# Performance work log

Hardware: AMD Instinct MI355X
Metric: run time of the kernel (lower is better)

## Reference

```python
import jax, jax.numpy as jnp
import numpy as np

EMBED_DIM = 768
N_HEADS = 12
TIME_RATIO = 0.5
HEAD_DIM = EMBED_DIM // N_HEADS          # 64
T_HEAD = int(HEAD_DIM * TIME_RATIO)      # 32 time dims per head
T_DIM = T_HEAD * N_HEADS                 # 384 time dims overall
EPS = 1e-5


def _ln(v, g, b):
    m = jnp.mean(v, axis=-1, keepdims=True)
    var = jnp.mean((v - m) ** 2, axis=-1, keepdims=True)
    return (v - m) * jax.lax.rsqrt(var + EPS) * g + b


def minkowski_ln(x, g_t, b_t, g_s, b_s):
    # normalize time-like and space-like channel groups separately
    xt, xs = x[..., :T_DIM], x[..., T_DIM:]
    return jnp.concatenate([_ln(xt, g_t, b_t), _ln(xs, g_s, b_s)], axis=-1)


def lorentz_attention(x, Wq, bq, Wk, bk, Wv, bv, Wo, bo):
    B, S, D = x.shape
    def heads(W, b):
        return (x @ W + b).reshape(B, S, N_HEADS, HEAD_DIM).transpose(0, 2, 1, 3)
    q, k, v = heads(Wq, bq), heads(Wk, bk), heads(Wv, bv)
    # Minkowski metric signature (-,...,-,+,...,+) within each head
    eta = jnp.concatenate([-jnp.ones((T_HEAD,), x.dtype), jnp.ones((HEAD_DIM - T_HEAD,), x.dtype)])
    logits = jnp.einsum('bhqd,bhkd->bhqk', q * eta, k) / np.sqrt(HEAD_DIM).astype(np.float32)
    attn = jax.nn.softmax(logits, axis=-1)
    o = jnp.einsum('bhqk,bhkd->bhqd', attn, v)
    o = o.transpose(0, 2, 1, 3).reshape(B, S, D)
    return o @ Wo + bo


def setup_inputs() -> dict:
    key = jax.random.key(0)
    ks = jax.random.split(key, 16)
    D, H4 = EMBED_DIM, EMBED_DIM * 4
    s = 0.02
    inp = {
        'x': jax.random.normal(ks[0], (2, 2048, D), jnp.float32),
        'Wq': jax.random.normal(ks[1], (D, D), jnp.float32) * s, 'bq': jnp.zeros((D,), jnp.float32),
        'Wk': jax.random.normal(ks[2], (D, D), jnp.float32) * s, 'bk': jnp.zeros((D,), jnp.float32),
        'Wv': jax.random.normal(ks[3], (D, D), jnp.float32) * s, 'bv': jnp.zeros((D,), jnp.float32),
        'Wo': jax.random.normal(ks[4], (D, D), jnp.float32) * s, 'bo': jnp.zeros((D,), jnp.float32),
        'g1t': jnp.ones((T_DIM,), jnp.float32), 'b1t': jnp.zeros((T_DIM,), jnp.float32),
        'g1s': jnp.ones((D - T_DIM,), jnp.float32), 'b1s': jnp.zeros((D - T_DIM,), jnp.float32),
        'W1': jax.random.normal(ks[5], (D, H4), jnp.float32) * s, 'bb1': jnp.zeros((H4,), jnp.float32),
        'W2': jax.random.normal(ks[6], (H4, D), jnp.float32) * s, 'bb2': jnp.zeros((D,), jnp.float32),
        'g2t': jnp.ones((T_DIM,), jnp.float32), 'b2t': jnp.zeros((T_DIM,), jnp.float32),
        'g2s': jnp.ones((D - T_DIM,), jnp.float32), 'b2s': jnp.zeros((D - T_DIM,), jnp.float32),
    }
    return inp


def reference(x, Wq, bq, Wk, bk, Wv, bv, Wo, bo,
              g1t, b1t, g1s, b1s, W1, bb1, W2, bb2,
              g2t, b2t, g2s, b2s):
    a = lorentz_attention(x, Wq, bq, Wk, bk, Wv, bv, Wo, bo)
    x = minkowski_ln(x + a, g1t, b1t, g1s, b1s)
    h = jax.nn.gelu(x @ W1 + bb1) @ W2 + bb2
    x = minkowski_ln(x + h, g2t, b2t, g2s, b2s)
    return x
```

## Files before the change

kernel.cpp:

```cpp
#include <hip/hip_runtime.h>
#include <cstddef>
#include <cstdint>

#define D_EMB  768
#define NHEAD  12
#define HDIM   64
#define THEAD  32
#define SEQ    2048
#define BATCH  2
#define NROW   (BATCH*SEQ)
#define HID4   3072

typedef unsigned short u16;
typedef __bf16 bf16x8 __attribute__((ext_vector_type(8)));
typedef float  f32x4  __attribute__((ext_vector_type(4)));
typedef unsigned short u16x8 __attribute__((ext_vector_type(8)));

__device__ __forceinline__ u16 f2bf(float f) {
    unsigned u = __builtin_bit_cast(unsigned, f);
    return (u16)((u + 0x7FFFu + ((u >> 16) & 1u)) >> 16);
}
__device__ __forceinline__ float bf2f(u16 h) {
    return __builtin_bit_cast(float, (unsigned)h << 16);
}

__device__ __forceinline__ void gload_lds16(const void* g, void* l) {
    __builtin_amdgcn_global_load_lds(
        reinterpret_cast<const __attribute__((address_space(1))) void*>(
            reinterpret_cast<uintptr_t>(g)),
        reinterpret_cast<__attribute__((address_space(3))) void*>(
            (uint32_t)reinterpret_cast<uintptr_t>(l)),
        16, 0, 0);
}

__global__ __launch_bounds__(256)
void cast_bf16(const float* __restrict__ in, u16* __restrict__ out, int n)
{
    const int i = (blockIdx.x * 256 + threadIdx.x) * 8;
    if (i >= n) return;
    const float4 a = *reinterpret_cast<const float4*>(in + i);
    const float4 b = *reinterpret_cast<const float4*>(in + i + 4);
    u16x8 h;
    h[0] = f2bf(a.x); h[1] = f2bf(a.y); h[2] = f2bf(a.z); h[3] = f2bf(a.w);
    h[4] = f2bf(b.x); h[5] = f2bf(b.y); h[6] = f2bf(b.z); h[7] = f2bf(b.w);
    *reinterpret_cast<u16x8*>(out + i) = h;
}

__global__ __launch_bounds__(256)
void concat_bias(const float* __restrict__ bq, const float* __restrict__ bk,
                 const float* __restrict__ bv, float* __restrict__ dst)
{
    const int i = blockIdx.x * 256 + threadIdx.x;
    if (i >= 2304) return;
    dst[i] = i < 768 ? bq[i] : (i < 1536 ? bk[i - 768] : bv[i - 1536]);
}

__global__ __launch_bounds__(256)
void transpose_cast(const float* __restrict__ W, u16* __restrict__ WT,
                    int K, int M)
{
    __shared__ float t[32][33];
    const int m0 = blockIdx.x * 32, k0 = blockIdx.y * 32;
    const int tx = threadIdx.x & 31, ty = threadIdx.x >> 5;
#pragma unroll
    for (int i = 0; i < 32; i += 8)
        t[ty + i][tx] = W[(size_t)(k0 + ty + i) * M + m0 + tx];
    __syncthreads();
#pragma unroll
    for (int i = 0; i < 32; i += 8)
        WT[(size_t)(m0 + ty + i) * K + k0 + tx] = f2bf(t[tx][ty + i]);
}

__global__ __launch_bounds__(256)
void transpose_cast4(const float* __restrict__ W0, const float* __restrict__ W1_,
                     const float* __restrict__ W2_, const float* __restrict__ W3_,
                     u16* __restrict__ WT)
{
    __shared__ float t[32][33];
    const int z = blockIdx.z;
    const float* W = z == 0 ? W0 : z == 1 ? W1_ : z == 2 ? W2_ : W3_;
    const int m0 = blockIdx.x * 32, k0 = blockIdx.y * 32;
    const int tx = threadIdx.x & 31, ty = threadIdx.x >> 5;
#pragma unroll
    for (int i = 0; i < 32; i += 8)
        t[ty + i][tx] = W[(size_t)(k0 + ty + i) * 768 + m0 + tx];
    __syncthreads();
#pragma unroll
    for (int i = 0; i < 32; i += 8)
        WT[(size_t)(z * 768 + m0 + ty + i) * 768 + k0 + tx] = f2bf(t[tx][ty + i]);
}

template<int EPI>
__global__ __launch_bounds__(256)
void gemm_bf16(const u16* __restrict__ A, const u16* __restrict__ B,
               const float* __restrict__ bias, void* __restrict__ Cp,
               u16* __restrict__ VTp, int K, int N)
{
    __shared__ u16 As[2][128 * 32];
    __shared__ u16 Bs[2][128 * 32];
    const int tid  = threadIdx.x;
    const int lane = tid & 63;
    const int w    = tid >> 6;
    const int m0 = blockIdx.x * 128, n0 = blockIdx.y * 128;
    const int wr = (w >> 1) << 6, wc = (w & 1) << 6;

    const int seg0 = (w << 11) + lane * 16;
    const int row0 = seg0 >> 6, cb0 = (seg0 & 63) >> 1;
    const int seg1 = seg0 + 1024;
    const int row1 = seg1 >> 6, cb1 = (seg1 & 63) >> 1;
    const u16* a0 = A + (size_t)(m0 + row0) * K + cb0;
    const u16* a1 = A + (size_t)(m0 + row1) * K + cb1;
    const u16* b0 = B + (size_t)(n0 + row0) * K + cb0;
    const u16* b1 = B + (size_t)(n0 + row1) * K + cb1;
    const int lo0 = (w * 2 + 0) << 9;
    const int lo1 = (w * 2 + 1) << 9;

    int aIdx[4], bIdx[4];
#pragma unroll
    for (int i = 0; i < 4; ++i) {
        aIdx[i] = (wr + i * 16 + (lane & 15)) * 32 + ((lane >> 4) << 3);
        bIdx[i] = (wc + i * 16 + (lane & 15)) * 32 + ((lane >> 4) << 3);
    }

    f32x4 acc[4][4];
#pragma unroll
    for (int i = 0; i < 4; ++i)
#pragma unroll
        for (int j = 0; j < 4; ++j)
#pragma unroll
            for (int q = 0; q < 4; ++q) acc[i][j][q] = 0.f;

    gload_lds16(a0, &As[0][lo0]);
    gload_lds16(a1, &As[0][lo1]);
    gload_lds16(b0, &Bs[0][lo0]);
    gload_lds16(b1, &Bs[0][lo1]);
    __syncthreads();

    int cur = 0;
    for (int k0 = 0; k0 < K; k0 += 32) {
        if (k0 + 32 < K) {
            gload_lds16(a0 + k0 + 32, &As[cur ^ 1][lo0]);
            gload_lds16(a1 + k0 + 32, &As[cur ^ 1][lo1]);
            gload_lds16(b0 + k0 + 32, &Bs[cur ^ 1][lo0]);
            gload_lds16(b1 + k0 + 32, &Bs[cur ^ 1][lo1]);
        }
        bf16x8 af[4], bv[4];
#pragma unroll
        for (int i = 0; i < 4; ++i)
            af[i] = *reinterpret_cast<const bf16x8*>(&As[cur][aIdx[i]]);
#pragma unroll
        for (int j = 0; j < 4; ++j)
            bv[j] = *reinterpret_cast<const bf16x8*>(&Bs[cur][bIdx[j]]);
#pragma unroll
        for (int i = 0; i < 4; ++i)
#pragma unroll
            for (int j = 0; j < 4; ++j)
                acc[i][j] = __builtin_amdgcn_mfma_f32_16x16x32_bf16(
                    af[i], bv[j], acc[i][j], 0, 0, 0);
        __syncthreads();
        cur ^= 1;
    }

#pragma unroll
    for (int i = 0; i < 4; ++i) {
#pragma unroll
        for (int q = 0; q < 4; ++q) {
            const int row = m0 + wr + i * 16 + ((lane >> 4) << 2) + q;
#pragma unroll
            for (int j = 0; j < 4; ++j) {
                const int col = n0 + wc + j * 16 + (lane & 15);
                float v = acc[i][j][q] + bias[col];
                if (EPI == 2) {
                    const float u3 = v * v * v;
                    v = 0.5f * v * (1.f + tanhf(0.7978845608028654f *
                                                (v + 0.044715f * u3)));
                }
                if (EPI == 0) {
                    ((float*)Cp)[(size_t)row * N + col] = v;
                } else if (EPI == 2) {
                    ((u16*)Cp)[(size_t)row * N + col] = f2bf(v);
                } else {
                    if (n0 < 1536) {
                        ((u16*)Cp)[(size_t)row * 1536 + col] = f2bf(v);
                    } else {
                        const int c2 = col - 1536;
                        const int hh = c2 >> 6, dd = c2 & 63;
                        const int bb = row >> 11, tok = row & 2047;
                        VTp[((size_t)(bb * NHEAD + hh) * HDIM + dd) * SEQ + tok]
                            = f2bf(v);
                    }
                }
            }
        }
    }
}

__global__ __launch_bounds__(256)
void gemm_n64(const u16* __restrict__ A, const u16* __restrict__ B,
              const float* __restrict__ bias, float* __restrict__ C,
              int K, int N)
{
    __shared__ u16 As[2][64 * 32];
    __shared__ u16 Bs[2][128 * 32];
    const int tid  = threadIdx.x;
    const int lane = tid & 63;
    const int w    = tid >> 6;
    const int l15  = lane & 15;
    const int g    = lane >> 4;
    const int m0 = blockIdx.x * 64, n0 = blockIdx.y * 128;

    const int segA = (w << 10) + lane * 16;
    const int rowA = segA >> 6, cbA = (segA & 63) >> 1;
    const u16* aP = A + (size_t)(m0 + rowA) * K + cbA;
    const int loA = w << 9;
    const int seg0 = (w << 11) + lane * 16;
    const int row0 = seg0 >> 6, cb0 = (seg0 & 63) >> 1;
    const int seg1 = seg0 + 1024;
    const int row1 = seg1 >> 6, cb1 = (seg1 & 63) >> 1;
    const u16* b0 = B + (size_t)(n0 + row0) * K + cb0;
    const u16* b1 = B + (size_t)(n0 + row1) * K + cb1;
    const int lo0 = w << 10, lo1 = (w << 10) + 512;

    int aIdx[4], bIdx[2];
#pragma unroll
    for (int i = 0; i < 4; ++i) aIdx[i] = (i * 16 + l15) * 32 + (g << 3);
#pragma unroll
    for (int j = 0; j < 2; ++j) bIdx[j] = ((w << 5) + j * 16 + l15) * 32 + (g << 3);

    f32x4 acc[4][2];
#pragma unroll
    for (int i = 0; i < 4; ++i)
#pragma unroll
        for (int j = 0; j < 2; ++j)
#pragma unroll
            for (int q = 0; q < 4; ++q) acc[i][j][q] = 0.f;

    gload_lds16(aP, &As[0][loA]);
    gload_lds16(b0, &Bs[0][lo0]);
    gload_lds16(b1, &Bs[0][lo1]);
    __syncthreads();

    int cur = 0;
    for (int k0 = 0; k0 < K; k0 += 32) {
        if (k0 + 32 < K) {
            gload_lds16(aP + k0 + 32, &As[cur ^ 1][loA]);
            gload_lds16(b0 + k0 + 32, &Bs[cur ^ 1][lo0]);
            gload_lds16(b1 + k0 + 32, &Bs[cur ^ 1][lo1]);
        }
        bf16x8 af[4], bv[2];
#pragma unroll
        for (int i = 0; i < 4; ++i)
            af[i] = *reinterpret_cast<const bf16x8*>(&As[cur][aIdx[i]]);
#pragma unroll
        for (int j = 0; j < 2; ++j)
            bv[j] = *reinterpret_cast<const bf16x8*>(&Bs[cur][bIdx[j]]);
#pragma unroll
        for (int i = 0; i < 4; ++i)
#pragma unroll
            for (int j = 0; j < 2; ++j)
                acc[i][j] = __builtin_amdgcn_mfma_f32_16x16x32_bf16(
                    af[i], bv[j], acc[i][j], 0, 0, 0);
        __syncthreads();
        cur ^= 1;
    }

#pragma unroll
    for (int i = 0; i < 4; ++i) {
#pragma unroll
        for (int q = 0; q < 4; ++q) {
            const int row = m0 + i * 16 + (g << 2) + q;
#pragma unroll
            for (int j = 0; j < 2; ++j) {
                const int col = n0 + (w << 5) + j * 16 + l15;
                C[(size_t)row * N + col] = acc[i][j][q] + bias[col];
            }
        }
    }
}

__global__ __launch_bounds__(256)
void attn_mfma(const u16* __restrict__ QK, const u16* __restrict__ VT,
               u16* __restrict__ O)
{
    __shared__ u16 Ks[2][64 * 64];
    __shared__ u16 Vs[2][64 * 64];
    __shared__ u16 Ps[64 * 72];

    const int tid  = threadIdx.x;
    const int lane = tid & 63;
    const int w    = tid >> 6;
    const int l15  = lane & 15;
    const int g    = lane >> 4;
    const int bh   = blockIdx.x;
    const int b    = bh / NHEAD, h = bh % NHEAD;
    const int q0   = blockIdx.y * 64;
    const int bS   = b * SEQ;

    bf16x8 aq[2];
    {
        const u16* Qg = QK + (size_t)(bS + q0 + (w << 4) + l15) * 1536 + h * HDIM;
#pragma unroll
        for (int kk = 0; kk < 2; ++kk) {
            u16x8 hq = *reinterpret_cast<const u16x8*>(Qg + kk * 32 + g * 8);
            if (kk == 0) {
#pragma unroll
                for (int j = 0; j < 8; ++j) hq[j] ^= 0x8000u;
            }
            aq[kk] = __builtin_bit_cast(bf16x8, hq);
        }
    }

    const int rl = lane >> 3;
    const int cs = (((lane & 7) ^ rl) << 3);
    const u16* pK = QK + (size_t)(bS + 16 * w + rl) * 1536 + 768 + h * HDIM + cs;
    const u16* pV = VT + ((size_t)(b * NHEAD + h) * HDIM + 16 * w + rl) * SEQ + cs;

    int swz[2];
#pragma unroll
    for (int kk = 0; kk < 2; ++kk)
        swz[kk] = ((kk * 4 + g) ^ (l15 & 7)) << 3;

    f32x4 accO[4];
#pragma unroll
    for (int n = 0; n < 4; ++n)
#pragma unroll
        for (int q = 0; q < 4; ++q) accO[n][q] = 0.f;
    float psum[4] = {0.f, 0.f, 0.f, 0.f};

#define ATTN_STAGE(c, kt)                                                   \
    do {                                                                    \
        u16* dK = &Ks[c][w * 1024];                                         \
        u16* dV = &Vs[c][w * 1024];                                         \
        gload_lds16(pK + (size_t)(kt) * 1536,     dK);                      \
        gload_lds16(pK + (size_t)((kt) + 8) * 1536, dK + 512);              \
        gload_lds16(pV + (kt),            dV);                              \
        gload_lds16(pV + (kt) + 8 * SEQ,  dV + 512);                        \
    } while (0)

    ATTN_STAGE(0, 0);
    __syncthreads();
    int cur = 0;

    for (int kt = 0; kt < SEQ; kt += 64) {
        if (kt + 64 < SEQ) ATTN_STAGE(cur ^ 1, kt + 64);

        f32x4 sac[4];
#pragma unroll
        for (int n = 0; n < 4; ++n) {
#pragma unroll
            for (int q = 0; q < 4; ++q) sac[n][q] = 0.f;
#pragma unroll
            for (int kk = 0; kk < 2; ++kk) {
                const bf16x8 bk = *reinterpret_cast<const bf16x8*>(
                    &Ks[cur][(n * 16 + l15) * 64 + swz[kk]]);
                sac[n] = __builtin_amdgcn_mfma_f32_16x16x32_bf16(
                    aq[kk], bk, sac[n], 0, 0, 0);
            }
        }

#pragma unroll
        for (int r4 = 0; r4 < 4; ++r4) {
            const int prow = (w << 4) + (g << 2) + r4;
#pragma unroll
            for (int n = 0; n < 4; ++n) {
                const float sv =
                    __builtin_amdgcn_exp2f(sac[n][r4] * 0.18033688011112042f);
                psum[r4] += sv;
                *(__bf16*)&Ps[prow * 72 + n * 16 + l15] = (__bf16)sv;
            }
        }

        bf16x8 pa[2];
#pragma unroll
        for (int kk = 0; kk < 2; ++kk)
            pa[kk] = *reinterpret_cast<const bf16x8*>(
                &Ps[((w << 4) + l15) * 72 + kk * 32 + g * 8]);
#pragma unroll
        for (int n = 0; n < 4; ++n) {
#pragma unroll
            for (int kk = 0; kk < 2; ++kk) {
                const bf16x8 bv = *reinterpret_cast<const bf16x8*>(
                    &Vs[cur][(n * 16 + l15) * 64 + swz[kk]]);
                accO[n] = __builtin_amdgcn_mfma_f32_16x16x32_bf16(
                    pa[kk], bv, accO[n], 0, 0, 0);
            }
        }
        __syncthreads();
        cur ^= 1;
    }

#pragma unroll
    for (int r4 = 0; r4 < 4; ++r4) {
        float ps = psum[r4];
#pragma unroll
        for (int off = 1; off < 16; off <<= 1)
            ps += __shfl_xor(ps, off, 16);
        const float inv = 1.f / ps;
        const int qr = q0 + (w << 4) + (g << 2) + r4;
#pragma unroll
        for (int n = 0; n < 4; ++n)
            O[(size_t)(bS + qr) * D_EMB + h * HDIM + n * 16 + l15]
                = f2bf(accO[n][r4] * inv);
    }
#undef ATTN_STAGE
}

__global__ __launch_bounds__(256)
void mink_ln(const float* __restrict__ X, const float* __restrict__ R,
             const float* __restrict__ gt, const float* __restrict__ bt,
             const float* __restrict__ gs, const float* __restrict__ bs,
             float* __restrict__ Out, u16* __restrict__ OutB, int nrows)
{
    const int wid  = (int)((blockIdx.x * 256 + threadIdx.x) >> 6);
    const int lane = threadIdx.x & 63;
    const int row  = wid >> 1, half = wid & 1;
    if (row >= nrows) return;

    const float* g  = half ? gs : gt;
    const float* bb = half ? bs : bt;
    const size_t base = (size_t)row * D_EMB + half * 384;

    float v[6];
    float sum = 0.f;
#pragma unroll
    for (int i = 0; i < 6; ++i) {
        const float t = X[base + i * 64 + lane] + R[base + i * 64 + lane];
        v[i] = t; sum += t;
    }
#pragma unroll
    for (int off = 32; off; off >>= 1) sum += __shfl_xor(sum, off);
    const float mean = sum * (1.f / 384.f);

    float ss = 0.f;
#pragma unroll
    for (int i = 0; i < 6; ++i) { const float d = v[i] - mean; ss += d * d; }
#pragma unroll
    for (int off = 32; off; off >>= 1) ss += __shfl_xor(ss, off);
    const float rstd = rsqrtf(ss * (1.f / 384.f) + 1e-5f);

#pragma unroll
    for (int i = 0; i < 6; ++i) {
        const int e = i * 64 + lane;
        const float o = (v[i] - mean) * rstd * g[e] + bb[e];
        Out[base + e] = o;
        if (OutB) OutB[base + e] = f2bf(o);
    }
}

extern "C" void kernel_launch(void* const* d_in, const int* in_sizes, int n_in,
                              void* d_out, int out_size, void* d_ws, size_t ws_size,
                              hipStream_t stream)
{
    const float* x   = (const float*)d_in[0];
    const float* Wq  = (const float*)d_in[1];
    const float* bq  = (const float*)d_in[2];
    const float* Wk  = (const float*)d_in[3];
    const float* bk  = (const float*)d_in[4];
    const float* Wv  = (const float*)d_in[5];
    const float* bv  = (const float*)d_in[6];
    const float* Wo  = (const float*)d_in[7];
    const float* bo  = (const float*)d_in[8];
    const float* g1t = (const float*)d_in[9];
    const float* b1t = (const float*)d_in[10];
    const float* g1s = (const float*)d_in[11];
    const float* b1s = (const float*)d_in[12];
    const float* W1  = (const float*)d_in[13];
    const float* bb1 = (const float*)d_in[14];
    const float* W2  = (const float*)d_in[15];
    const float* bb2 = (const float*)d_in[16];
    const float* g2t = (const float*)d_in[17];
    const float* b2t = (const float*)d_in[18];
    const float* g2s = (const float*)d_in[19];
    const float* b2s = (const float*)d_in[20];
    float* out = (float*)d_out;

    const size_t ND = (size_t)NROW * D_EMB;
    u16* WqkvoT = (u16*)d_ws;
    u16* W1T = WqkvoT + 2359296;
    u16* W2T = W1T + 2359296;
    u16* xb  = W2T + 2359296;
    u16* QKb = xb + ND;
    u16* VTb = QKb + (size_t)NROW * 1536;
    u16* Ab  = VTb + ND;
    u16* Hb  = QKb;
    float* AoF  = (float*)(Ab + ND);
    float* bqkv = AoF;
    float* X1   = AoF + ND;

    const dim3 blk(256);

    cast_bf16<<<1536, blk, 0, stream>>>(x, xb, (int)ND);
    concat_bias<<<9, blk, 0, stream>>>(bq, bk, bv, bqkv);
    transpose_cast4<<<dim3(24, 24, 4), blk, 0, stream>>>(Wq, Wk, Wv, Wo, WqkvoT);
    transpose_cast<<<dim3(96, 24), blk, 0, stream>>>(W1, W1T, 768, 3072);
    transpose_cast<<<dim3(24, 96), blk, 0, stream>>>(W2, W2T, 3072, 768);

    gemm_bf16<3><<<dim3(32, 18), blk, 0, stream>>>(xb, WqkvoT, bqkv, QKb, VTb,
                                                   768, 2304);
    attn_mfma<<<dim3(BATCH * NHEAD, SEQ / 64), blk, 0, stream>>>(QKb, VTb, Ab);

    gemm_n64<<<dim3(64, 6), blk, 0, stream>>>(Ab, WqkvoT + (size_t)2304 * 768,
                                              bo, AoF, 768, 768);
    mink_ln<<<2048, blk, 0, stream>>>(x, AoF, g1t, b1t, g1s, b1s, X1, xb, NROW);
    gemm_bf16<2><<<dim3(32, 24), blk, 0, stream>>>(xb, W1T, bb1, Hb, nullptr,
                                                   768, 3072);
    gemm_n64<<<dim3(64, 6), blk, 0, stream>>>(Hb, W2T, bb2, AoF, 3072, 768);
    mink_ln<<<2048, blk, 0, stream>>>(X1, AoF, g2t, b2t, g2s, b2s, out, nullptr, NROW);
}
```

Before: 209.7 us.

## Merge prep kernels and give attention waves two query tiles each

Five preprocessing launches (x cast, bias concat, three weight transposes) become one kernel that dispatches on block index. The attention kernel now runs 2 waves per 64-query block, each wave owning 32 query rows. Each K/V fragment loaded from LDS therefore feeds two MFMAs. P is written as packed 4-element stores, and the QKV GEMM writes V^T with the token order permuted within each 64-token group to match that layout. Costs are higher register pressure from doubled accumulators and fewer waves per block to hide latency.

```diff
diff --git a/kernel.cpp b/kernel.cpp
--- a/kernel.cpp
+++ b/kernel.cpp
@@ -20,9 +20,6 @@
     unsigned u = __builtin_bit_cast(unsigned, f);
     return (u16)((u + 0x7FFFu + ((u >> 16) & 1u)) >> 16);
 }
-__device__ __forceinline__ float bf2f(u16 h) {
-    return __builtin_bit_cast(float, (unsigned)h << 16);
-}
 
 __device__ __forceinline__ void gload_lds16(const void* g, void* l) {
     __builtin_amdgcn_global_load_lds(
@@ -33,34 +30,11 @@
         16, 0, 0);
 }
 
-__global__ __launch_bounds__(256)
-void cast_bf16(const float* __restrict__ in, u16* __restrict__ out, int n)
-{
-    const int i = (blockIdx.x * 256 + threadIdx.x) * 8;
-    if (i >= n) return;
-    const float4 a = *reinterpret_cast<const float4*>(in + i);
-    const float4 b = *reinterpret_cast<const float4*>(in + i + 4);
-    u16x8 h;
-    h[0] = f2bf(a.x); h[1] = f2bf(a.y); h[2] = f2bf(a.z); h[3] = f2bf(a.w);
-    h[4] = f2bf(b.x); h[5] = f2bf(b.y); h[6] = f2bf(b.z); h[7] = f2bf(b.w);
-    *reinterpret_cast<u16x8*>(out + i) = h;
-}
-
-__global__ __launch_bounds__(256)
-void concat_bias(const float* __restrict__ bq, const float* __restrict__ bk,
-                 const float* __restrict__ bv, float* __restrict__ dst)
-{
-    const int i = blockIdx.x * 256 + threadIdx.x;
-    if (i >= 2304) return;
-    dst[i] = i < 768 ? bq[i] : (i < 1536 ? bk[i - 768] : bv[i - 1536]);
-}
-
-__global__ __launch_bounds__(256)
-void transpose_cast(const float* __restrict__ W, u16* __restrict__ WT,
-                    int K, int M)
-{
-    __shared__ float t[32][33];
-    const int m0 = blockIdx.x * 32, k0 = blockIdx.y * 32;
+__device__ __forceinline__ void tcast(float (*t)[33], const float* __restrict__ W,
+                                      u16* __restrict__ WT, int K, int M,
+                                      int mt, int kt)
+{
+    const int m0 = mt * 32, k0 = kt * 32;
     const int tx = threadIdx.x & 31, ty = threadIdx.x >> 5;
 #pragma unroll
     for (int i = 0; i < 32; i += 8)
@@ -72,22 +46,40 @@
 }
 
 __global__ __launch_bounds__(256)
-void transpose_cast4(const float* __restrict__ W0, const float* __restrict__ W1_,
-                     const float* __restrict__ W2_, const float* __restrict__ W3_,
-                     u16* __restrict__ WT)
+void prep(const float* __restrict__ Wq, const float* __restrict__ Wk,
+          const float* __restrict__ Wv, const float* __restrict__ Wo,
+          const float* __restrict__ W1, const float* __restrict__ W2,
+          const float* __restrict__ bq, const float* __restrict__ bk,
+          const float* __restrict__ bv, const float* __restrict__ x,
+          u16* __restrict__ WqkvoT, u16* __restrict__ W1T,
+          u16* __restrict__ W2T, u16* __restrict__ xb,
+          float* __restrict__ bqkv)
 {
     __shared__ float t[32][33];
-    const int z = blockIdx.z;
-    const float* W = z == 0 ? W0 : z == 1 ? W1_ : z == 2 ? W2_ : W3_;
-    const int m0 = blockIdx.x * 32, k0 = blockIdx.y * 32;
-    const int tx = threadIdx.x & 31, ty = threadIdx.x >> 5;
-#pragma unroll
-    for (int i = 0; i < 32; i += 8)
-        t[ty + i][tx] = W[(size_t)(k0 + ty + i) * 768 + m0 + tx];
-    __syncthreads();
-#pragma unroll
-    for (int i = 0; i < 32; i += 8)
-        WT[(size_t)(z * 768 + m0 + ty + i) * 768 + k0 + tx] = f2bf(t[tx][ty + i]);
+    const int bid = blockIdx.x;
+    if (bid < 2304) {
+        const int z = bid / 576, r = bid % 576;
+        const float* W = z == 0 ? Wq : z == 1 ? Wk : z == 2 ? Wv : Wo;
+        tcast(t, W, WqkvoT + (size_t)z * 768 * 768, 768, 768, r % 24, r / 24);
+    } else if (bid < 4608) {
+        const int r = bid - 2304;
+        tcast(t, W1, W1T, 768, 3072, r % 96, r / 96);
+    } else if (bid < 6912) {
+        const int r = bid - 4608;
+        tcast(t, W2, W2T, 3072, 768, r % 24, r / 24);
+    } else if (bid < 8448) {
+        const int i = (bid - 6912) * 2048 + threadIdx.x * 8;
+        const float4 a = *reinterpret_cast<const float4*>(x + i);
+        const float4 b = *reinterpret_cast<const float4*>(x + i + 4);
+        u16x8 h;
+        h[0] = f2bf(a.x); h[1] = f2bf(a.y); h[2] = f2bf(a.z); h[3] = f2bf(a.w);
+        h[4] = f2bf(b.x); h[5] = f2bf(b.y); h[6] = f2bf(b.z); h[7] = f2bf(b.w);
+        *reinterpret_cast<u16x8*>(xb + i) = h;
+    } else {
+        const int i = (bid - 8448) * 256 + threadIdx.x;
+        if (i < 2304)
+            bqkv[i] = i < 768 ? bq[i] : (i < 1536 ? bk[i - 768] : bv[i - 1536]);
+    }
 }
 
 template<int EPI>
@@ -174,10 +166,6 @@
                     const float u3 = v * v * v;
                     v = 0.5f * v * (1.f + tanhf(0.7978845608028654f *
                                                 (v + 0.044715f * u3)));
-                }
-                if (EPI == 0) {
-                    ((float*)Cp)[(size_t)row * N + col] = v;
-                } else if (EPI == 2) {
                     ((u16*)Cp)[(size_t)row * N + col] = f2bf(v);
                 } else {
                     if (n0 < 1536) {
@@ -186,8 +174,10 @@
                         const int c2 = col - 1536;
                         const int hh = c2 >> 6, dd = c2 & 63;
                         const int bb = row >> 11, tok = row & 2047;
-                        VTp[((size_t)(bb * NHEAD + hh) * HDIM + dd) * SEQ + tok]
-                            = f2bf(v);
+                        const int t = tok & 63;
+                        const int p = ((t & 15) << 2) | (t >> 4);
+                        VTp[((size_t)(bb * NHEAD + hh) * HDIM + dd) * SEQ
+                            + (tok & ~63) + p] = f2bf(v);
                     }
                 }
             }
@@ -278,7 +268,7 @@
     }
 }
 
-__global__ __launch_bounds__(256)
+__global__ __launch_bounds__(128)
 void attn_mfma(const u16* __restrict__ QK, const u16* __restrict__ VT,
                u16* __restrict__ O)
 {
@@ -296,9 +286,11 @@
     const int q0   = blockIdx.y * 64;
     const int bS   = b * SEQ;
 
-    bf16x8 aq[2];
-    {
-        const u16* Qg = QK + (size_t)(bS + q0 + (w << 4) + l15) * 1536 + h * HDIM;
+    bf16x8 aq[2][2];
+#pragma unroll
+    for (int qb = 0; qb < 2; ++qb) {
+        const u16* Qg = QK + (size_t)(bS + q0 + w * 32 + qb * 16 + l15) * 1536
+                        + h * HDIM;
 #pragma unroll
         for (int kk = 0; kk < 2; ++kk) {
             u16x8 hq = *reinterpret_cast<const u16x8*>(Qg + kk * 32 + g * 8);
@@ -306,35 +298,38 @@
 #pragma unroll
                 for (int j = 0; j < 8; ++j) hq[j] ^= 0x8000u;
             }
-            aq[kk] = __builtin_bit_cast(bf16x8, hq);
+            aq[qb][kk] = __builtin_bit_cast(bf16x8, hq);
         }
     }
 
     const int rl = lane >> 3;
-    const int cs = (((lane & 7) ^ rl) << 3);
-    const u16* pK = QK + (size_t)(bS + 16 * w + rl) * 1536 + 768 + h * HDIM + cs;
-    const u16* pV = VT + ((size_t)(b * NHEAD + h) * HDIM + 16 * w + rl) * SEQ + cs;
+    const int cs = ((lane & 7) ^ rl) << 3;
+    const u16* pK = QK + (size_t)(bS + w * 32 + rl) * 1536 + 768 + h * HDIM + cs;
+    const u16* pV = VT + ((size_t)(b * NHEAD + h) * HDIM + w * 32 + rl) * SEQ + cs;
 
     int swz[2];
 #pragma unroll
     for (int kk = 0; kk < 2; ++kk)
         swz[kk] = ((kk * 4 + g) ^ (l15 & 7)) << 3;
 
-    f32x4 accO[4];
-#pragma unroll
-    for (int n = 0; n < 4; ++n)
-#pragma unroll
-        for (int q = 0; q < 4; ++q) accO[n][q] = 0.f;
-    float psum[4] = {0.f, 0.f, 0.f, 0.f};
-
-#define ATTN_STAGE(c, kt)                                                   \
-    do {                                                                    \
-        u16* dK = &Ks[c][w * 1024];                                         \
-        u16* dV = &Vs[c][w * 1024];                                         \
-        gload_lds16(pK + (size_t)(kt) * 1536,     dK);                      \
-        gload_lds16(pK + (size_t)((kt) + 8) * 1536, dK + 512);              \
-        gload_lds16(pV + (kt),            dV);                              \
-        gload_lds16(pV + (kt) + 8 * SEQ,  dV + 512);                        \
+    f32x4 accO[2][4];
+#pragma unroll
+    for (int qb = 0; qb < 2; ++qb)
+#pragma unroll
+        for (int n = 0; n < 4; ++n)
+#pragma unroll
+            for (int q = 0; q < 4; ++q) accO[qb][n][q] = 0.f;
+    float psum[2][4] = {};
+
+#define ATTN_STAGE(c, kt)                                                    \
+    do {                                                                     \
+        u16* dK = &Ks[c][w * 2048];                                          \
+        u16* dV = &Vs[c][w * 2048];                                          \
+        _Pragma("unroll")                                                    \
+        for (int i = 0; i < 4; ++i) {                                        \
+            gload_lds16(pK + (size_t)((kt) + 8 * i) * 1536, dK + 512 * i);   \
+            gload_lds16(pV + (size_t)(8 * i) * SEQ + (kt),  dV + 512 * i);   \
+        }                                                                    \
     } while (0)
 
     ATTN_STAGE(0, 0);
@@ -344,64 +339,83 @@
     for (int kt = 0; kt < SEQ; kt += 64) {
         if (kt + 64 < SEQ) ATTN_STAGE(cur ^ 1, kt + 64);
 
-        f32x4 sac[4];
-#pragma unroll
-        for (int n = 0; n < 4; ++n) {
-#pragma unroll
-            for (int q = 0; q < 4; ++q) sac[n][q] = 0.f;
-#pragma unroll
-            for (int kk = 0; kk < 2; ++kk) {
-                const bf16x8 bk = *reinterpret_cast<const bf16x8*>(
+        bf16x8 bk[4][2];
+#pragma unroll
+        for (int n = 0; n < 4; ++n)
+#pragma unroll
+            for (int kk = 0; kk < 2; ++kk)
+                bk[n][kk] = *reinterpret_cast<const bf16x8*>(
                     &Ks[cur][(n * 16 + l15) * 64 + swz[kk]]);
-                sac[n] = __builtin_amdgcn_mfma_f32_16x16x32_bf16(
-                    aq[kk], bk, sac[n], 0, 0, 0);
+
+        f32x4 sac[2][4];
+#pragma unroll
+        for (int qb = 0; qb < 2; ++qb)
+#pragma unroll
+            for (int n = 0; n < 4; ++n) {
+#pragma unroll
+                for (int q = 0; q < 4; ++q) sac[qb][n][q] = 0.f;
+#pragma unroll
+                for (int kk = 0; kk < 2; ++kk)
+                    sac[qb][n] = __builtin_amdgcn_mfma_f32_16x16x32_bf16(
+                        aq[qb][kk], bk[n][kk], sac[qb][n], 0, 0, 0);
             }
-        }
-
-#pragma unroll
-        for (int r4 = 0; r4 < 4; ++r4) {
-            const int prow = (w << 4) + (g << 2) + r4;
-#pragma unroll
-            for (int n = 0; n < 4; ++n) {
-                const float sv =
-                    __builtin_amdgcn_exp2f(sac[n][r4] * 0.18033688011112042f);
-                psum[r4] += sv;
-                *(__bf16*)&Ps[prow * 72 + n * 16 + l15] = (__bf16)sv;
+
+#pragma unroll
+        for (int qb = 0; qb < 2; ++qb)
+#pragma unroll
+            for (int r4 = 0; r4 < 4; ++r4) {
+                const int prow = w * 32 + qb * 16 + g * 4 + r4;
+                ushort4 pk4;
+                float sv0 = __builtin_amdgcn_exp2f(sac[qb][0][r4] * 0.18033688011112042f);
+                float sv1 = __builtin_amdgcn_exp2f(sac[qb][1][r4] * 0.18033688011112042f);
+                float sv2 = __builtin_amdgcn_exp2f(sac[qb][2][r4] * 0.18033688011112042f);
+                float sv3 = __builtin_amdgcn_exp2f(sac[qb][3][r4] * 0.18033688011112042f);
+                psum[qb][r4] += sv0 + sv1 + sv2 + sv3;
+                pk4.x = f2bf(sv0); pk4.y = f2bf(sv1);
+                pk4.z = f2bf(sv2); pk4.w = f2bf(sv3);
+                *reinterpret_cast<ushort4*>(&Ps[prow * 72 + (l15 << 2)]) = pk4;
             }
-        }
-
-        bf16x8 pa[2];
-#pragma unroll
-        for (int kk = 0; kk < 2; ++kk)
-            pa[kk] = *reinterpret_cast<const bf16x8*>(
-                &Ps[((w << 4) + l15) * 72 + kk * 32 + g * 8]);
-#pragma unroll
-        for (int n = 0; n < 4; ++n) {
-#pragma unroll
-            for (int kk = 0; kk < 2; ++kk) {
-                const bf16x8 bv = *reinterpret_cast<const bf16x8*>(
+
+        bf16x8 bv[4][2];
+#pragma unroll
+        for (int n = 0; n < 4; ++n)
+#pragma unroll
+            for (int kk = 0; kk < 2; ++kk)
+                bv[n][kk] = *reinterpret_cast<const bf16x8*>(
                     &Vs[cur][(n * 16 + l15) * 64 + swz[kk]]);
-                accO[n] = __builtin_amdgcn_mfma_f32_16x16x32_bf16(
-                    pa[kk], bv, accO[n], 0, 0, 0);
-            }
+#pragma unroll
+        for (int qb = 0; qb < 2; ++qb) {
+            bf16x8 pa[2];
+#pragma unroll
+            for (int kk = 0; kk < 2; ++kk)
+                pa[kk] = *reinterpret_cast<const bf16x8*>(
+                    &Ps[(w * 32 + qb * 16 + l15) * 72 + kk * 32 + g * 8]);
+#pragma unroll
+            for (int n = 0; n < 4; ++n)
+#pragma unroll
+                for (int kk = 0; kk < 2; ++kk)
+                    accO[qb][n] = __builtin_amdgcn_mfma_f32_16x16x32_bf16(
+                        pa[kk], bv[n][kk], accO[qb][n], 0, 0, 0);
         }
         __syncthreads();
         cur ^= 1;
     }
 
 #pragma unroll
-    for (int r4 = 0; r4 < 4; ++r4) {
-        float ps = psum[r4];
-#pragma unroll
-        for (int off = 1; off < 16; off <<= 1)
-            ps += __shfl_xor(ps, off, 16);
-        const float inv = 1.f / ps;
-        const int qr = q0 + (w << 4) + (g << 2) + r4;
-#pragma unroll
-        for (int n = 0; n < 4; ++n)
-            O[(size_t)(bS + qr) * D_EMB + h * HDIM + n * 16 + l15]
-                = f2bf(accO[n][r4] * inv);
-    }
+    for (int qb = 0; qb < 2; ++qb)
+#pragma unroll
+        for (int r4 = 0; r4 < 4; ++r4) {
+            float ps = psum[qb][r4];
+#pragma unroll
+            for (int off = 1; off < 16; off <<= 1)
+                ps += __shfl_xor(ps, off, 16);
+            const float inv = 1.f / ps;
+            const int qr = q0 + w * 32 + qb * 16 + g * 4 + r4;
+#pragma unroll
+            for (int n = 0; n < 4; ++n)
+                O[(size_t)(bS + qr) * D_EMB + h * HDIM + n * 16 + l15]
+                    = f2bf(accO[qb][n][r4] * inv);
+        }
 #undef ATTN_STAGE
 }
 
@@ -489,15 +503,12 @@
 
     const dim3 blk(256);
 
-    cast_bf16<<<1536, blk, 0, stream>>>(x, xb, (int)ND);
-    concat_bias<<<9, blk, 0, stream>>>(bq, bk, bv, bqkv);
-    transpose_cast4<<<dim3(24, 24, 4), blk, 0, stream>>>(Wq, Wk, Wv, Wo, WqkvoT);
-    transpose_cast<<<dim3(96, 24), blk, 0, stream>>>(W1, W1T, 768, 3072);
-    transpose_cast<<<dim3(24, 96), blk, 0, stream>>>(W2, W2T, 3072, 768);
+    prep<<<8457, blk, 0, stream>>>(Wq, Wk, Wv, Wo, W1, W2, bq, bk, bv, x,
+                                   WqkvoT, W1T, W2T, xb, bqkv);
 
     gemm_bf16<3><<<dim3(32, 18), blk, 0, stream>>>(xb, WqkvoT, bqkv, QKb, VTb,
                                                    768, 2304);
-    attn_mfma<<<dim3(BATCH * NHEAD, SEQ / 64), blk, 0, stream>>>(QKb, VTb, Ab);
+    attn_mfma<<<dim3(BATCH * NHEAD, SEQ / 64), dim3(128), 0, stream>>>(QKb, VTb, Ab);
 
     gemm_n64<<<dim3(64, 6), blk, 0, stream>>>(Ab, WqkvoT + (size_t)2304 * 768,
                                               bo, AoF, 768, 768);
```

After: 209.0 us. Within noise of the previous version (-0.3%).
